# Performance work log

Measured on AMD Instinct MI355X. Metric: run time of the kernel, lower is better.

## Reference

```python
import jax, jax.numpy as jnp
import numpy as np

DELTA = 1.5
EPS = 1e-7  # torch-em dice_score denominator clamp


def shift2d(t, off):
    # Equivalent to torch-em ReplicationPad + slice on the (already inverted)
    # offset: shifted[..., i, j] = t[..., clip(i + oy, 0, H-1), clip(j + ox, 0, W-1)]
    H, W = t.shape[-2], t.shape[-1]
    iy = jnp.clip(jnp.arange(H) + off[0], 0, H - 1)
    ix = jnp.clip(jnp.arange(W) + off[1], 0, W - 1)
    return t[..., iy, :][..., ix]


def dice_score_invert_sum(inp, tgt):
    # torch-em dice_score(invert=True, channelwise=True): channel axis = dim 1,
    # flatten everything else, sum of (1 - 2*num/den) over channels.
    num = jnp.einsum('bchw,bchw->c', inp, tgt)
    den = jnp.einsum('bchw,bchw->c', inp, inp) + jnp.einsum('bchw,bchw->c', tgt, tgt)
    score = 2.0 * num / jnp.maximum(den, EPS)
    return jnp.sum(1.0 - score)


def setup_inputs() -> dict:
    key = jax.random.key(0)
    k1, k2, k3 = jax.random.split(key, 3)
    B, E, H, W = 4, 12, 512, 512
    n_samples = 8
    input_ = jax.random.normal(k1, (B, E, H, W), dtype=jnp.float32)
    target = jax.random.randint(k2, (B, 1, H, W), 0, 50, dtype=jnp.int32)
    # offsets ~ randint(orange[0], orange[1]) per dim, i.e. values in [-27, -1]
    offsets = jax.random.randint(k3, (n_samples, 2), -27, 0, dtype=jnp.int32)
    return {"input_": input_, "target": target, "offsets": offsets}


def reference(input_, target, offsets):
    tgt = target.astype(jnp.float32)

    # embeddings -> affinities
    shifted_emb = jax.vmap(lambda o: shift2d(input_, o))(offsets)      # [S,B,E,H,W]
    ss = jnp.sum((input_[None] - shifted_emb) ** 2, axis=2)            # [S,B,H,W]
    norm = jnp.where(ss > 0, jnp.sqrt(jnp.where(ss > 0, ss, 1.0)), 0.0)
    affs = jnp.clip((2.0 * DELTA - norm) / (2.0 * DELTA), 0.0) ** 2
    affs = 1.0 - jnp.transpose(affs, (1, 0, 2, 3))                     # [B,S,H,W]

    # segmentation -> affinities
    shifted_seg = jax.vmap(lambda o: shift2d(tgt, o))(offsets)         # [S,B,1,H,W]
    target_affs = (tgt[None] == shifted_seg).astype(jnp.float32)[:, :, 0]
    target_affs = 1.0 - jnp.transpose(target_affs, (1, 0, 2, 3))       # [B,S,H,W]

    return dice_score_invert_sum(affs, target_affs)
```

## Files before the change

### kernel.cpp

```cpp
#include <hip/hip_runtime.h>


typedef float f2 __attribute__((ext_vector_type(2)));
typedef float f4 __attribute__((ext_vector_type(4)));

#define HWSZ   262144
#define NE     12
#define NC     13
#define NS     8
#define TROWS  16
#define TCOLS  128
#define NBLK   512
#define HROWS  44
#define HCOLS  156
#define HSZ    (HROWS * HCOLS)
#define NCHUNK (HCOLS / 4)
#define NSLOT  (HSZ / 4)

__global__ __launch_bounds__(512) void affloss_main(
    const float* __restrict__ emb, const int* __restrict__ seg,
    const int* __restrict__ offs, float* __restrict__ partial) {
  __shared__ f4 buf4[NSLOT];
  __shared__ float red[8][16];
  float* buf = (float*)buf4;

  const int bid = blockIdx.x;
  const int nb  = (bid & 7) * (NBLK / 8) + (bid >> 3);
  const int b   = nb >> 7;
  const int rem = nb & 127;
  const int r0  = (rem >> 2) * TROWS;
  const int c0  = (rem & 3) * TCOLS;

  const int tid = threadIdx.x;
  const int tx  = tid & 63;
  const int wv  = tid >> 6;

  const float* embB = emb + (size_t)b * NE * HWSZ;
  const int*   segB = seg + (size_t)b * HWSZ;

  int oyv[NS], oxv[NS];
  #pragma unroll
  for (int s = 0; s < NS; ++s) { oyv[s] = offs[2 * s]; oxv[s] = offs[2 * s + 1]; }

  int srow[4], sgc[4];
  #pragma unroll
  for (int k = 0; k < 4; ++k) {
    const int slot = tid + k * 512;
    const int rr = slot / NCHUNK;
    const int ch = slot - rr * NCHUNK;
    int gr = r0 - 28 + rr; gr = gr < 0 ? 0 : gr;
    srow[k] = gr;
    sgc[k] = c0 - 28 + 4 * ch;
  }
  const bool s3 = tid < (NSLOT - 3 * 512);

  auto stage_load = [&](int e, f4* r) {
    const float* p = (e < NE) ? (embB + (size_t)e * HWSZ) : (const float*)segB;
    #pragma unroll
    for (int k = 0; k < 4; ++k) {
      if (k == 3 && !s3) continue;
      const float* rowp = p + srow[k] * 512;
      if (sgc[k] >= 0) {
        r[k] = *reinterpret_cast<const f4*>(rowp + sgc[k]);
      } else {
        const float v = rowp[0];
        r[k] = f4{v, v, v, v};
      }
    }
  };
  auto stage_write = [&](const f4* r) {
    #pragma unroll
    for (int k = 0; k < 4; ++k) {
      if (k == 3 && !s3) continue;
      buf4[tid + k * 512] = r[k];
    }
  };

  f2 ssv[2][NS];
  #pragma unroll
  for (int q = 0; q < 2; ++q)
    #pragma unroll
    for (int s = 0; s < NS; ++s) ssv[q][s] = f2{0.f, 0.f};
  float numa[NS], dena[NS];
  #pragma unroll
  for (int s = 0; s < NS; ++s) { numa[s] = 0.f; dena[s] = 0.f; }

  f4 r[4];
  stage_load(0, r);

  for (int e = 0; e < NC; ++e) {
    __syncthreads();
    stage_write(r);
    __syncthreads();
    if (e + 1 < NC) stage_load(e + 1, r);

    if (e < NE) {
      #pragma unroll
      for (int q = 0; q < 2; ++q) {
        const int hr = wv + 8 * q + 28;
        const int cb = hr * HCOLS + 28 + 2 * tx;
        const f2 cc = *reinterpret_cast<const f2*>(&buf[cb]);
        #pragma unroll
        for (int s = 0; s < NS; ++s) {
          const int a = cb + oyv[s] * HCOLS + oxv[s];
          f2 sh; sh[0] = buf[a]; sh[1] = buf[a + 1];
          const f2 d = cc - sh;
          ssv[q][s][0] = fmaf(d[0], d[0], ssv[q][s][0]);
          ssv[q][s][1] = fmaf(d[1], d[1], ssv[q][s][1]);
        }
      }
    } else {
      #pragma unroll
      for (int q = 0; q < 2; ++q) {
        const int hr = wv + 8 * q + 28;
        const int cb = hr * HCOLS + 28 + 2 * tx;
        const int tc0 = __float_as_int(buf[cb]);
        const int tc1 = __float_as_int(buf[cb + 1]);
        #pragma unroll
        for (int s = 0; s < NS; ++s) {
          const int a = cb + oyv[s] * HCOLS + oxv[s];
          const int t0 = __float_as_int(buf[a]);
          const int t1 = __float_as_int(buf[a + 1]);
          {
            const float n  = __builtin_amdgcn_sqrtf(ssv[q][s][0]);
            const float rc = fmaxf(fmaf(n, -(1.0f / 3.0f), 1.0f), 0.0f);
            const float A  = fmaf(-rc, rc, 1.0f);
            const float ta = (tc0 == t0) ? 0.f : 1.f;
            numa[s] = fmaf(A, ta, numa[s]);
            dena[s] += fmaf(A, A, ta);
          }
          {
            const float n  = __builtin_amdgcn_sqrtf(ssv[q][s][1]);
            const float rc = fmaxf(fmaf(n, -(1.0f / 3.0f), 1.0f), 0.0f);
            const float A  = fmaf(-rc, rc, 1.0f);
            const float ta = (tc1 == t1) ? 0.f : 1.f;
            numa[s] = fmaf(A, ta, numa[s]);
            dena[s] += fmaf(A, A, ta);
          }
        }
      }
    }
  }

  float arr[16];
  #pragma unroll
  for (int s = 0; s < NS; ++s) { arr[s] = numa[s]; arr[8 + s] = dena[s]; }
  #pragma unroll
  for (int k = 0; k < 16; ++k) {
    float v = arr[k];
    #pragma unroll
    for (int o = 32; o > 0; o >>= 1) v += __shfl_down(v, o, 64);
    arr[k] = v;
  }
  const int lane = tid & 63;
  if (lane == 0) {
    #pragma unroll
    for (int k = 0; k < 16; ++k) red[wv][k] = arr[k];
  }
  __syncthreads();
  if (tid < 16) {
    float v = 0.f;
    #pragma unroll
    for (int w = 0; w < 8; ++w) v += red[w][tid];
    partial[tid * NBLK + blockIdx.x] = v;
  }
}

__global__ __launch_bounds__(1024) void affloss_final(
    const float* __restrict__ partial, float* __restrict__ out) {
  __shared__ double csum[16];
  const int lane = threadIdx.x & 63, wv = threadIdx.x >> 6;

  double s = 0.0;
  for (int i = lane; i < NBLK; i += 64)
    s += (double)partial[wv * NBLK + i];
  #pragma unroll
  for (int o = 32; o > 0; o >>= 1) s += __shfl_down(s, o, 64);
  if (lane == 0) csum[wv] = s;
  __syncthreads();

  if (threadIdx.x == 0) {
    double total = 0.0;
    #pragma unroll
    for (int c = 0; c < 8; ++c) {
      double num = csum[c];
      double den = csum[8 + c];
      if (den < 1e-7) den = 1e-7;
      total += 1.0 - 2.0 * num / den;
    }
    out[0] = (float)total;
  }
}

extern "C" void kernel_launch(void* const* d_in, const int* in_sizes, int n_in,
                              void* d_out, int out_size, void* d_ws, size_t ws_size,
                              hipStream_t stream) {
  const float* emb  = (const float*)d_in[0];
  const int*   seg  = (const int*)d_in[1];
  const int*   offs = (const int*)d_in[2];
  float* partial = (float*)d_ws;

  affloss_main<<<NBLK, 512, 0, stream>>>(emb, seg, offs, partial);
  affloss_final<<<1, 1024, 0, stream>>>(partial, (float*)d_out);
}
```

Baseline: 41.88 us.

## Halve tile width, double blocks, and double-buffer shared staging per channel

New measurement: 67.10 us. +60.2%, slower.

```diff
diff --git a/kernel.cpp b/kernel.cpp
--- a/kernel.cpp
+++ b/kernel.cpp
@@ -9,10 +9,10 @@
 #define NC     13
 #define NS     8
 #define TROWS  16
-#define TCOLS  128
-#define NBLK   512
+#define TCOLS  64
+#define NBLK   1024
 #define HROWS  44
-#define HCOLS  156
+#define HCOLS  92
 #define HSZ    (HROWS * HCOLS)
 #define NCHUNK (HCOLS / 4)
 #define NSLOT  (HSZ / 4)
@@ -20,46 +20,47 @@
 __global__ __launch_bounds__(512) void affloss_main(
     const float* __restrict__ emb, const int* __restrict__ seg,
     const int* __restrict__ offs, float* __restrict__ partial) {
-  __shared__ f4 buf4[NSLOT];
+  __shared__ f4 buf4[2][NSLOT];
   __shared__ float red[8][16];
-  float* buf = (float*)buf4;
 
   const int bid = blockIdx.x;
   const int nb  = (bid & 7) * (NBLK / 8) + (bid >> 3);
-  const int b   = nb >> 7;
-  const int rem = nb & 127;
-  const int r0  = (rem >> 2) * TROWS;
-  const int c0  = (rem & 3) * TCOLS;
+  const int b   = nb >> 8;
+  const int rem = nb & 255;
+  const int r0  = (rem >> 3) * TROWS;
+  const int c0  = (rem & 7) * TCOLS;
 
   const int tid = threadIdx.x;
-  const int tx  = tid & 63;
+  const int tx  = tid & 31;
+  const int row = tid >> 5;
   const int wv  = tid >> 6;
 
   const float* embB = emb + (size_t)b * NE * HWSZ;
   const int*   segB = seg + (size_t)b * HWSZ;
 
-  int oyv[NS], oxv[NS];
+  int soff[NS];
   #pragma unroll
-  for (int s = 0; s < NS; ++s) { oyv[s] = offs[2 * s]; oxv[s] = offs[2 * s + 1]; }
+  for (int s = 0; s < NS; ++s)
+    soff[s] = offs[2 * s] * HCOLS + offs[2 * s + 1];
 
-  int srow[4], sgc[4];
+  int srow[2], sgc[2];
   #pragma unroll
-  for (int k = 0; k < 4; ++k) {
+  for (int k = 0; k < 2; ++k) {
     const int slot = tid + k * 512;
     const int rr = slot / NCHUNK;
     const int ch = slot - rr * NCHUNK;
     int gr = r0 - 28 + rr; gr = gr < 0 ? 0 : gr;
-    srow[k] = gr;
+    srow[k] = gr * 512;
     sgc[k] = c0 - 28 + 4 * ch;
   }
-  const bool s3 = tid < (NSLOT - 3 * 512);
+  const bool has1 = tid < (NSLOT - 512);
 
   auto stage_load = [&](int e, f4* r) {
     const float* p = (e < NE) ? (embB + (size_t)e * HWSZ) : (const float*)segB;
     #pragma unroll
-    for (int k = 0; k < 4; ++k) {
-      if (k == 3 && !s3) continue;
-      const float* rowp = p + srow[k] * 512;
+    for (int k = 0; k < 2; ++k) {
+      if (k == 1 && !has1) continue;
+      const float* rowp = p + srow[k];
       if (sgc[k] >= 0) {
         r[k] = *reinterpret_cast<const f4*>(rowp + sgc[k]);
       } else {
@@ -68,77 +69,68 @@
       }
     }
   };
-  auto stage_write = [&](const f4* r) {
-    #pragma unroll
-    for (int k = 0; k < 4; ++k) {
-      if (k == 3 && !s3) continue;
-      buf4[tid + k * 512] = r[k];
-    }
+  auto stage_write = [&](int bi, const f4* r) {
+    buf4[bi][tid] = r[0];
+    if (has1) buf4[bi][tid + 512] = r[1];
   };
 
-  f2 ssv[2][NS];
+  f2 ssv[NS];
   #pragma unroll
-  for (int q = 0; q < 2; ++q)
-    #pragma unroll
-    for (int s = 0; s < NS; ++s) ssv[q][s] = f2{0.f, 0.f};
+  for (int s = 0; s < NS; ++s) ssv[s] = f2{0.f, 0.f};
   float numa[NS], dena[NS];
+
+  const int cb = (row + 28) * HCOLS + 28 + 2 * tx;
+
+  f4 r[2];
+  stage_load(0, r);
+  stage_write(0, r);
+  __syncthreads();
+
   #pragma unroll
-  for (int s = 0; s < NS; ++s) { numa[s] = 0.f; dena[s] = 0.f; }
-
-  f4 r[4];
-  stage_load(0, r);
-
   for (int e = 0; e < NC; ++e) {
-    __syncthreads();
-    stage_write(r);
-    __syncthreads();
     if (e + 1 < NC) stage_load(e + 1, r);
+    const float* bufp = (const float*)buf4[e & 1];
 
     if (e < NE) {
+      const f2 cc = *reinterpret_cast<const f2*>(bufp + cb);
       #pragma unroll
-      for (int q = 0; q < 2; ++q) {
-        const int hr = wv + 8 * q + 28;
-        const int cb = hr * HCOLS + 28 + 2 * tx;
-        const f2 cc = *reinterpret_cast<const f2*>(&buf[cb]);
-        #pragma unroll
-        for (int s = 0; s < NS; ++s) {
-          const int a = cb + oyv[s] * HCOLS + oxv[s];
-          f2 sh; sh[0] = buf[a]; sh[1] = buf[a + 1];
-          const f2 d = cc - sh;
-          ssv[q][s][0] = fmaf(d[0], d[0], ssv[q][s][0]);
-          ssv[q][s][1] = fmaf(d[1], d[1], ssv[q][s][1]);
-        }
+      for (int s = 0; s < NS; ++s) {
+        const int a = cb + soff[s];
+        f2 sh; sh[0] = bufp[a]; sh[1] = bufp[a + 1];
+        const f2 d = cc - sh;
+        ssv[s][0] = fmaf(d[0], d[0], ssv[s][0]);
+        ssv[s][1] = fmaf(d[1], d[1], ssv[s][1]);
       }
     } else {
+      const int tc0 = __float_as_int(bufp[cb]);
+      const int tc1 = __float_as_int(bufp[cb + 1]);
       #pragma unroll
-      for (int q = 0; q < 2; ++q) {
-        const int hr = wv + 8 * q + 28;
-        const int cb = hr * HCOLS + 28 + 2 * tx;
-        const int tc0 = __float_as_int(buf[cb]);
-        const int tc1 = __float_as_int(buf[cb + 1]);
-        #pragma unroll
-        for (int s = 0; s < NS; ++s) {
-          const int a = cb + oyv[s] * HCOLS + oxv[s];
-          const int t0 = __float_as_int(buf[a]);
-          const int t1 = __float_as_int(buf[a + 1]);
-          {
-            const float n  = __builtin_amdgcn_sqrtf(ssv[q][s][0]);
-            const float rc = fmaxf(fmaf(n, -(1.0f / 3.0f), 1.0f), 0.0f);
-            const float A  = fmaf(-rc, rc, 1.0f);
-            const float ta = (tc0 == t0) ? 0.f : 1.f;
-            numa[s] = fmaf(A, ta, numa[s]);
-            dena[s] += fmaf(A, A, ta);
-          }
-          {
-            const float n  = __builtin_amdgcn_sqrtf(ssv[q][s][1]);
-            const float rc = fmaxf(fmaf(n, -(1.0f / 3.0f), 1.0f), 0.0f);
-            const float A  = fmaf(-rc, rc, 1.0f);
-            const float ta = (tc1 == t1) ? 0.f : 1.f;
-            numa[s] = fmaf(A, ta, numa[s]);
-            dena[s] += fmaf(A, A, ta);
-          }
+      for (int s = 0; s < NS; ++s) {
+        const int a = cb + soff[s];
+        const int t0 = __float_as_int(bufp[a]);
+        const int t1 = __float_as_int(bufp[a + 1]);
+        float nacc = 0.f, dacc = 0.f;
+        {
+          const float n  = __builtin_amdgcn_sqrtf(ssv[s][0]);
+          const float rc = fmaxf(fmaf(n, -(1.0f / 3.0f), 1.0f), 0.0f);
+          const float A  = fmaf(-rc, rc, 1.0f);
+          const float ta = (tc0 == t0) ? 0.f : 1.f;
+          nacc = fmaf(A, ta, nacc); dacc += fmaf(A, A, ta);
         }
+        {
+          const float n  = __builtin_amdgcn_sqrtf(ssv[s][1]);
+          const float rc = fmaxf(fmaf(n, -(1.0f / 3.0f), 1.0f), 0.0f);
+          const float A  = fmaf(-rc, rc, 1.0f);
+          const float ta = (tc1 == t1) ? 0.f : 1.f;
+          nacc = fmaf(A, ta, nacc); dacc += fmaf(A, A, ta);
+        }
+        numa[s] = nacc; dena[s] = dacc;
       }
+    }
+
+    if (e + 1 < NC) {
+      stage_write((e + 1) & 1, r);
+      __syncthreads();
     }
   }
 
@@ -153,6 +145,7 @@
     arr[k] = v;
   }
   const int lane = tid & 63;
+  __syncthreads();
   if (lane == 0) {
     #pragma unroll
     for (int k = 0; k < 16; ++k) red[wv][k] = arr[k];
```
